# Kernel tuning notes

Measured on AMD Instinct MI355X. Metric: run time of the kernel, lower is better.

The kernel has to match this reference:

```python
import jax, jax.numpy as jnp
import numpy as np

D_MODEL = 1024
N_HEADS = 16
HEAD_DIM = D_MODEL // N_HEADS
BS, SEQ = 4, 2048


def setup_inputs() -> dict:
    key = jax.random.key(0)
    ks = jax.random.split(key, 12)
    s = 1.0 / np.sqrt(D_MODEL)
    inp = {
        'query': jax.random.normal(ks[0], (BS, SEQ, D_MODEL), jnp.float32),
        'key_in': jax.random.normal(ks[1], (BS, SEQ, D_MODEL), jnp.float32),
        'value': jax.random.normal(ks[2], (BS, SEQ, D_MODEL), jnp.float32),
        'mask': jax.random.randint(ks[3], (BS, SEQ, SEQ), 0, 2, jnp.int32),
        'wq_w': jax.random.uniform(ks[4], (D_MODEL, D_MODEL), jnp.float32, -s, s),
        'wq_b': jax.random.uniform(ks[5], (D_MODEL,), jnp.float32, -s, s),
        'wk_w': jax.random.uniform(ks[6], (D_MODEL, D_MODEL), jnp.float32, -s, s),
        'wk_b': jax.random.uniform(ks[7], (D_MODEL,), jnp.float32, -s, s),
        'wv_w': jax.random.uniform(ks[8], (D_MODEL, D_MODEL), jnp.float32, -s, s),
        'wv_b': jax.random.uniform(ks[9], (D_MODEL,), jnp.float32, -s, s),
        'fc_w': jax.random.uniform(ks[10], (D_MODEL, D_MODEL), jnp.float32, -s, s),
        'fc_b': jax.random.uniform(ks[11], (D_MODEL,), jnp.float32, -s, s),
    }
    return inp


def _split_heads(x):
    # [B, S, D] -> [B, H, S, Dh]
    b, s, _ = x.shape
    return x.reshape(b, s, N_HEADS, HEAD_DIM).transpose(0, 2, 1, 3)


def reference(query, key_in, value, mask,
              wq_w, wq_b, wk_w, wk_b, wv_w, wv_b, fc_w, fc_b):
    # torch Linear: y = x @ W.T + b
    q = _split_heads(query @ wq_w.T + wq_b)   # [B,H,S,Dh]
    k = _split_heads(key_in @ wk_w.T + wk_b)
    v = _split_heads(value @ wv_w.T + wv_b)

    scale = 1.0 / np.sqrt(HEAD_DIM).astype(np.float32)
    scores = jnp.einsum('bhqd,bhkd->bhqk', q, k) * scale  # [B,H,S,S]
    m = (mask[:, None, :, :] == 0)
    scores = jnp.where(m, jnp.float32(-1e9), scores)
    attn = jax.nn.softmax(scores, axis=-1)
    out = jnp.einsum('bhqk,bhkd->bhqd', attn, v)           # [B,H,S,Dh]
    out = out.transpose(0, 2, 1, 3).reshape(query.shape[0], query.shape[1], D_MODEL)
    return out @ fc_w.T + fc_b
```

## Files before the change

### kernel.cpp

```cpp
#include <hip/hip_runtime.h>
#include <hip/hip_bf16.h>


typedef __attribute__((ext_vector_type(8))) short bf16x8;
typedef __attribute__((ext_vector_type(4))) float f32x4;
typedef unsigned int u32;
typedef unsigned short u16;
typedef unsigned long long u64;

#define SEQ 2048
#define DM 1024
#define NH 16
#define HD 64

__device__ __forceinline__ u16 f2bf(float f) {
  __hip_bfloat16 h = __float2bfloat16(f);
  return __builtin_bit_cast(u16, h);
}
__device__ __forceinline__ u32 pack2(float a, float b) {
  return (u32)f2bf(a) | ((u32)f2bf(b) << 16);
}
__device__ __forceinline__ float max3f(float a, float b, float c) {
  return fmaxf(fmaxf(a, b), c);
}

typedef __attribute__((address_space(3))) u32 lds_u32;
typedef const __attribute__((address_space(1))) u32 gbl_u32;
__device__ __forceinline__ void gll16(const void* g, void* l) {
  __builtin_amdgcn_global_load_lds((gbl_u32*)g, (lds_u32*)l, 16, 0, 0);
}

__global__ __launch_bounds__(256) void cast_all(
    const float* __restrict__ q, const float* __restrict__ k, const float* __restrict__ v,
    const float* __restrict__ wq, const float* __restrict__ wk,
    const float* __restrict__ wv, const float* __restrict__ wf,
    u16* __restrict__ dst)
{
  int i4 = blockIdx.x * 256 + threadIdx.x;
  const float* s; int rel;
  if      (i4 < 2097152) { s = q;  rel = i4;           }
  else if (i4 < 4194304) { s = k;  rel = i4 - 2097152; }
  else if (i4 < 6291456) { s = v;  rel = i4 - 4194304; }
  else if (i4 < 6553600) { s = wq; rel = i4 - 6291456; }
  else if (i4 < 6815744) { s = wk; rel = i4 - 6553600; }
  else if (i4 < 7077888) { s = wv; rel = i4 - 6815744; }
  else                   { s = wf; rel = i4 - 7077888; }
  float4 val = ((const float4*)s)[rel];
  uint2 o; o.x = pack2(val.x, val.y); o.y = pack2(val.z, val.w);
  ((uint2*)dst)[i4] = o;
}

__global__ __launch_bounds__(256) void maskbits(const int* __restrict__ mask, u32* __restrict__ bm) {
  int t = blockIdx.x * 256 + threadIdx.x;
  int v = mask[t];
  u64 bal = __ballot(v != 0);
  if ((threadIdx.x & 63) == 0) {
    bm[(t >> 5)]     = (u32)bal;
    bm[(t >> 5) + 1] = (u32)(bal >> 32);
  }
}

template<int MODE>
__global__ __launch_bounds__(256) void gemm_bt(
    const u16* __restrict__ Pm, const u16* __restrict__ Pn,
    const float* __restrict__ bias, void* __restrict__ outp, float scale)
{
  __shared__ alignas(16) u16 Al[128 * 32];
  __shared__ alignas(16) u16 Bl[128 * 32];
  const int tid = threadIdx.x;
  const int l = tid & 63;
  const int wv = tid >> 6;
  const int lane15 = l & 15, g = l >> 4;
  const int wr = wv >> 1, wc = wv & 1;
  const int mBase = blockIdx.y * 128, nBase = blockIdx.x * 128;

  f32x4 acc[4][4];
#pragma unroll
  for (int a = 0; a < 4; ++a)
#pragma unroll
    for (int b = 0; b < 4; ++b) acc[a][b] = (f32x4){0.f, 0.f, 0.f, 0.f};

  const int srow = tid >> 2, skc = tid & 3;
  const u16* gA = Pm + (size_t)(mBase + srow) * 1024 + skc * 8;
  const u16* gB = Pn + (size_t)(nBase + srow) * 1024 + skc * 8;

  for (int kt = 0; kt < 32; ++kt) {
    __syncthreads();
    const u16* a0 = gA + kt * 32;
    const u16* b0 = gB + kt * 32;
    gll16(a0,             &Al[tid * 8]);
    gll16(a0 + 64 * 1024, &Al[(tid + 256) * 8]);
    gll16(b0,             &Bl[tid * 8]);
    gll16(b0 + 64 * 1024, &Bl[(tid + 256) * 8]);
    __syncthreads();
    bf16x8 af[4], bff[4];
#pragma unroll
    for (int mt = 0; mt < 4; ++mt)
      af[mt] = *(const bf16x8*)&Al[(wr * 64 + mt * 16 + lane15) * 32 + g * 8];
#pragma unroll
    for (int nt = 0; nt < 4; ++nt)
      bff[nt] = *(const bf16x8*)&Bl[(wc * 64 + nt * 16 + lane15) * 32 + g * 8];
#pragma unroll
    for (int mt = 0; mt < 4; ++mt)
#pragma unroll
      for (int nt = 0; nt < 4; ++nt)
        acc[mt][nt] = __builtin_amdgcn_mfma_f32_16x16x32_bf16(af[mt], bff[nt], acc[mt][nt], 0, 0, 0);
  }

#pragma unroll
  for (int mt = 0; mt < 4; ++mt) {
    const int mi = mBase + wr * 64 + mt * 16 + g * 4;
#pragma unroll
    for (int nt = 0; nt < 4; ++nt) {
      const int ni = nBase + wc * 64 + nt * 16 + lane15;
      f32x4 v = acc[mt][nt];
      if constexpr (MODE == 0) {
        f32x4 bb = *(const f32x4*)&bias[mi];
        int b = ni >> 11, s = ni & 2047;
        int h = mi >> 6, dh = mi & 63;
        uint2 w;
        w.x = pack2((v[0] + bb[0]) * scale, (v[1] + bb[1]) * scale);
        w.y = pack2((v[2] + bb[2]) * scale, (v[3] + bb[3]) * scale);
        *(uint2*)&((u16*)outp)[((size_t)((b << 4) + h) * SEQ + s) * HD + dh] = w;
      } else if constexpr (MODE == 1) {
        float bv = bias[ni];
        int b = mi >> 11, s = mi & 2047;
        int h = ni >> 6, dh = ni & 63;
        uint2 w;
        w.x = pack2(v[0] + bv, v[1] + bv);
        w.y = pack2(v[2] + bv, v[3] + bv);
        *(uint2*)&((u16*)outp)[((size_t)((b << 4) + h) * HD + dh) * SEQ + s] = w;
      } else {
        f32x4 bb = *(const f32x4*)&bias[mi];
        f32x4 w = v + bb;
        *(f32x4*)&((float*)outp)[(size_t)ni * 1024 + mi] = w;
      }
    }
  }
}

__global__ __launch_bounds__(256) void attn_kernel(
    const u16* __restrict__ Qb, const u16* __restrict__ Kb,
    const u16* __restrict__ Vt, const u32* __restrict__ bm,
    u16* __restrict__ AO)
{
  __shared__ alignas(16) u16 Kl[2][64 * 64];
  __shared__ alignas(16) u16 Vl[2][64 * 64];
  __shared__ uint2 Pl[4][256];
  const int bid = blockIdx.x;
  const int bh = (bid & 7) * 8 + ((bid >> 3) & 7);
  const int qt = bid >> 6;
  const int b = bh >> 4, h = bh & 15;
  const int tid = threadIdx.x;
  const int wv = tid >> 6, l = tid & 63;
  const int q16 = l & 15, g = l >> 4;
  const int lr = l >> 3, lc = l & 7;
  const int sx = q16 & 7;

  const u16* Qp = Qb + (size_t)bh * SEQ * HD;
  const u16* Kp = Kb + (size_t)bh * SEQ * HD;
  const u16* Vp = Vt + (size_t)bh * HD * SEQ;
  const int qrow = qt * 64 + wv * 16;

  const bf16x8 qf0 = *(const bf16x8*)&Qp[(qrow + q16) * HD + g * 8];
  const bf16x8 qf1 = *(const bf16x8*)&Qp[(qrow + q16) * HD + 32 + g * 8];
  const u32* bmq = bm + (size_t)(b * SEQ + qrow + q16) * (SEQ / 32);

  const int i0 = wv * 2;
  const u16* ksrc0 = Kp + (size_t)((i0 + 0) * 8 + lr) * HD + (lc ^ lr) * 8;
  const u16* ksrc1 = Kp + (size_t)((i0 + 1) * 8 + lr) * HD + (lc ^ lr) * 8;
  const u16* vsrc0 = Vp + (size_t)((i0 + 0) * 8 + lr) * SEQ + (lc ^ lr) * 8;
  const u16* vsrc1 = Vp + (size_t)((i0 + 1) * 8 + lr) * SEQ + (lc ^ lr) * 8;

  union { u32 u[4]; bf16x8 v; } ones;
  ones.u[0] = ones.u[1] = ones.u[2] = ones.u[3] = 0x3F803F80u;

  float mrun = 8.0f;
  f32x4 accO[4], accSum;
#pragma unroll
  for (int dt = 0; dt < 4; ++dt) accO[dt] = (f32x4){0.f, 0.f, 0.f, 0.f};
  accSum = (f32x4){0.f, 0.f, 0.f, 0.f};
  const f32x4 z = {0.f, 0.f, 0.f, 0.f};

  {
    gll16(ksrc0, &Kl[0][(i0 + 0) * 512 + l * 8]);
    gll16(ksrc1, &Kl[0][(i0 + 1) * 512 + l * 8]);
    gll16(vsrc0, &Vl[0][(i0 + 0) * 512 + l * 8]);
    gll16(vsrc1, &Vl[0][(i0 + 1) * 512 + l * 8]);
  }

  for (int kb = 0; kb < SEQ / 64; ++kb) {
    const int cur = kb & 1;
    const u32 w0 = bmq[kb * 2], w1 = bmq[kb * 2 + 1];
    if (kb < SEQ / 64 - 1) {
      const int nxt = cur ^ 1;
      const size_t ko = (size_t)(kb + 1) * 64;
      gll16(ksrc0 + ko * HD, &Kl[nxt][(i0 + 0) * 512 + l * 8]);
      gll16(ksrc1 + ko * HD, &Kl[nxt][(i0 + 1) * 512 + l * 8]);
      gll16(vsrc0 + ko,      &Vl[nxt][(i0 + 0) * 512 + l * 8]);
      gll16(vsrc1 + ko,      &Vl[nxt][(i0 + 1) * 512 + l * 8]);
      asm volatile("s_waitcnt vmcnt(4)" ::: "memory");
    } else {
      asm volatile("s_waitcnt vmcnt(0)" ::: "memory");
    }
    __builtin_amdgcn_s_barrier();
    __builtin_amdgcn_sched_barrier(0);

    const u16* Kc = &Kl[cur][0];
    const u16* Vc = &Vl[cur][0];

    f32x4 accS[4];
    __builtin_amdgcn_s_setprio(1);
#pragma unroll
    for (int n = 0; n < 4; ++n) {
      const int rk = n * 16 + q16;
      bf16x8 kf0 = *(const bf16x8*)&Kc[rk * 64 + ((g ^ sx) * 8)];
      bf16x8 kf1 = *(const bf16x8*)&Kc[rk * 64 + (((4 + g) ^ sx) * 8)];
      accS[n] = __builtin_amdgcn_mfma_f32_16x16x32_bf16(kf0, qf0, z, 0, 0, 0);
      accS[n] = __builtin_amdgcn_mfma_f32_16x16x32_bf16(kf1, qf1, accS[n], 0, 0, 0);
    }
    __builtin_amdgcn_s_setprio(0);

    float s[16];
#pragma unroll
    for (int n = 0; n < 4; ++n) {
      const u32 nib = ((n & 2) ? w1 : w0) >> ((n & 1) * 16 + g * 4);
#pragma unroll
      for (int r = 0; r < 4; ++r)
        s[n * 4 + r] = ((nib >> r) & 1u) ? accS[n][r] : -1e9f;
    }
    float pmax;
    {
      float g0 = max3f(s[0],  s[1],  s[2]);
      float g1 = max3f(s[3],  s[4],  s[5]);
      float g2 = max3f(s[6],  s[7],  s[8]);
      float g3 = max3f(s[9],  s[10], s[11]);
      float g4 = max3f(s[12], s[13], s[14]);
      pmax = max3f(max3f(g0, g1, g2), max3f(g3, g4, s[15]), -INFINITY);
    }
    pmax = fmaxf(pmax, __shfl_xor(pmax, 16));
    pmax = fmaxf(pmax, __shfl_xor(pmax, 32));

    if (!__all(pmax - mrun <= 12.0f)) {
      const float mnew = fmaxf(mrun, pmax);
      const float alpha = exp2f(mrun - mnew);
      accSum[0] *= alpha;
#pragma unroll
      for (int dt = 0; dt < 4; ++dt) {
        accO[dt][0] *= alpha; accO[dt][1] *= alpha;
        accO[dt][2] *= alpha; accO[dt][3] *= alpha;
      }
      mrun = mnew;
    }

    u16 pb[16];
#pragma unroll
    for (int i = 0; i < 16; ++i)
      pb[i] = f2bf(exp2f(s[i] - mrun));

#pragma unroll
    for (int n = 0; n < 4; ++n) {
      uint2 pw;
      pw.x = (u32)pb[n * 4 + 0] | ((u32)pb[n * 4 + 1] << 16);
      pw.y = (u32)pb[n * 4 + 2] | ((u32)pb[n * 4 + 3] << 16);
      Pl[wv][q16 * 16 + ((n * 4 + g) ^ q16)] = pw;
    }
#pragma unroll
    for (int ch = 0; ch < 2; ++ch) {
      const int u0 = ch * 8 + g * 2;
      uint2 lo = Pl[wv][q16 * 16 + ((u0 + 0) ^ q16)];
      uint2 hi = Pl[wv][q16 * 16 + ((u0 + 1) ^ q16)];
      union { u32 u[4]; bf16x8 v; } pf;
      pf.u[0] = lo.x; pf.u[1] = lo.y; pf.u[2] = hi.x; pf.u[3] = hi.y;
      __builtin_amdgcn_s_setprio(1);
#pragma unroll
      for (int dt = 0; dt < 4; ++dt) {
        const int rv = dt * 16 + q16;
        bf16x8 vf = *(const bf16x8*)&Vc[rv * 64 + (((ch * 4 + g) ^ sx) * 8)];
        accO[dt] = __builtin_amdgcn_mfma_f32_16x16x32_bf16(vf, pf.v, accO[dt], 0, 0, 0);
      }
      accSum = __builtin_amdgcn_mfma_f32_16x16x32_bf16(ones.v, pf.v, accSum, 0, 0, 0);
      __builtin_amdgcn_s_setprio(0);
    }
    __builtin_amdgcn_s_barrier();
  }

  const float inv = 1.f / fmaxf(accSum[0], 1e-37f);
#pragma unroll
  for (int dt = 0; dt < 4; ++dt) {
    uint2 o;
    o.x = pack2(accO[dt][0] * inv, accO[dt][1] * inv);
    o.y = pack2(accO[dt][2] * inv, accO[dt][3] * inv);
    *(uint2*)&AO[(size_t)(b * SEQ + qrow + q16) * DM + h * HD + dt * 16 + g * 4] = o;
  }
}

extern "C" void kernel_launch(void* const* d_in, const int* in_sizes, int n_in,
                              void* d_out, int out_size, void* d_ws, size_t ws_size,
                              hipStream_t stream) {
  const float* q  = (const float*)d_in[0];
  const float* k  = (const float*)d_in[1];
  const float* v  = (const float*)d_in[2];
  const int* mask = (const int*)d_in[3];
  const float* wq = (const float*)d_in[4];
  const float* bq = (const float*)d_in[5];
  const float* wk = (const float*)d_in[6];
  const float* bk = (const float*)d_in[7];
  const float* wv = (const float*)d_in[8];
  const float* bv = (const float*)d_in[9];
  const float* wf = (const float*)d_in[10];
  const float* bf = (const float*)d_in[11];

  u16* XQ = (u16*)d_ws;
  u16* XK = XQ + 8388608;
  u16* XV = XK + 8388608;
  u16* WQ = XV + 8388608;
  u16* WK = WQ + 1048576;
  u16* WV = WK + 1048576;
  u16* WF = WV + 1048576;
  u16* QB = WF + 1048576;
  u16* KB = QB + 8388608;
  u16* VT = KB + 8388608;
  u32* BM = (u32*)(VT + 8388608);
  u16* AO = XQ;

  const float qscale = 0.125f * 1.44269504088896f;

  cast_all<<<28672, 256, 0, stream>>>(q, k, v, wq, wk, wv, wf, XQ);
  maskbits<<<65536, 256, 0, stream>>>(mask, BM);
  gemm_bt<0><<<dim3(64, 8), 256, 0, stream>>>(WQ, XQ, bq, QB, qscale);
  gemm_bt<0><<<dim3(64, 8), 256, 0, stream>>>(WK, XK, bk, KB, 1.0f);
  gemm_bt<1><<<dim3(8, 64), 256, 0, stream>>>(XV, WV, bv, VT, 1.0f);
  attn_kernel<<<2048, 256, 0, stream>>>(QB, KB, VT, BM, AO);
  gemm_bt<2><<<dim3(64, 8), 256, 0, stream>>>(WF, AO, bf, (float*)d_out, 1.0f);
}
```

Measured before the change: 487.7 us.

## Batch QKV projections into one launch, use packed bf16 convert, trim attention loop

Merges the three Q/K/V projection GEMMs into one launch with a z-dimension selecting operands, and splits the output projection into its own kernel. Float-to-bf16 conversion now uses a single packed v_cvt_pk_bf16_f32 instruction. The attention loop drops its s_setprio calls, works on the score accumulators in place, advances K/V source pointers incrementally, and adds an occupancy hint to launch bounds. The aim is fewer launches, better GPU fill during projections, and fewer conversion and address instructions, at the cost of possible register-pressure or scheduling changes.

```diff
diff --git a/kernel.cpp b/kernel.cpp
--- a/kernel.cpp
+++ b/kernel.cpp
@@ -13,12 +13,10 @@
 #define NH 16
 #define HD 64
 
-__device__ __forceinline__ u16 f2bf(float f) {
-  __hip_bfloat16 h = __float2bfloat16(f);
-  return __builtin_bit_cast(u16, h);
-}
 __device__ __forceinline__ u32 pack2(float a, float b) {
-  return (u32)f2bf(a) | ((u32)f2bf(b) << 16);
+  u32 d;
+  asm("v_cvt_pk_bf16_f32 %0, %1, %2" : "=v"(d) : "v"(a), "v"(b));
+  return d;
 }
 __device__ __forceinline__ float max3f(float a, float b, float c) {
   return fmaxf(fmaxf(a, b), c);
@@ -60,19 +58,26 @@
   }
 }
 
-template<int MODE>
-__global__ __launch_bounds__(256) void gemm_bt(
-    const u16* __restrict__ Pm, const u16* __restrict__ Pn,
-    const float* __restrict__ bias, void* __restrict__ outp, float scale)
+__global__ __launch_bounds__(256) void gemm_qkv(
+    const u16* __restrict__ WQp, const u16* __restrict__ XQp, const float* __restrict__ bq,
+    const u16* __restrict__ WKp, const u16* __restrict__ XKp, const float* __restrict__ bk,
+    const u16* __restrict__ WVp, const u16* __restrict__ XVp, const float* __restrict__ bv,
+    u16* __restrict__ QB, u16* __restrict__ KB, u16* __restrict__ VT, float qscale)
 {
   __shared__ alignas(16) u16 Al[128 * 32];
   __shared__ alignas(16) u16 Bl[128 * 32];
+  const int z = blockIdx.z;
+  const u16 *Pm, *Pn; const float* bias;
+  int mBase, nBase;
+  if (z == 0)      { Pm = WQp; Pn = XQp; bias = bq; mBase = blockIdx.y * 128; nBase = blockIdx.x * 128; }
+  else if (z == 1) { Pm = WKp; Pn = XKp; bias = bk; mBase = blockIdx.y * 128; nBase = blockIdx.x * 128; }
+  else             { Pm = XVp; Pn = WVp; bias = bv; mBase = blockIdx.x * 128; nBase = blockIdx.y * 128; }
+
   const int tid = threadIdx.x;
   const int l = tid & 63;
   const int wv = tid >> 6;
   const int lane15 = l & 15, g = l >> 4;
   const int wr = wv >> 1, wc = wv & 1;
-  const int mBase = blockIdx.y * 128, nBase = blockIdx.x * 128;
 
   f32x4 acc[4][4];
 #pragma unroll
@@ -107,39 +112,105 @@
         acc[mt][nt] = __builtin_amdgcn_mfma_f32_16x16x32_bf16(af[mt], bff[nt], acc[mt][nt], 0, 0, 0);
   }
 
-#pragma unroll
-  for (int mt = 0; mt < 4; ++mt) {
-    const int mi = mBase + wr * 64 + mt * 16 + g * 4;
-#pragma unroll
-    for (int nt = 0; nt < 4; ++nt) {
-      const int ni = nBase + wc * 64 + nt * 16 + lane15;
-      f32x4 v = acc[mt][nt];
-      if constexpr (MODE == 0) {
-        f32x4 bb = *(const f32x4*)&bias[mi];
+  if (z <= 1) {
+    const float scale = (z == 0) ? qscale : 1.0f;
+    u16* outp = (z == 0) ? QB : KB;
+#pragma unroll
+    for (int mt = 0; mt < 4; ++mt) {
+      const int mi = mBase + wr * 64 + mt * 16 + g * 4;
+      f32x4 bb = *(const f32x4*)&bias[mi];
+#pragma unroll
+      for (int nt = 0; nt < 4; ++nt) {
+        const int ni = nBase + wc * 64 + nt * 16 + lane15;
+        f32x4 v = acc[mt][nt];
         int b = ni >> 11, s = ni & 2047;
         int h = mi >> 6, dh = mi & 63;
         uint2 w;
         w.x = pack2((v[0] + bb[0]) * scale, (v[1] + bb[1]) * scale);
         w.y = pack2((v[2] + bb[2]) * scale, (v[3] + bb[3]) * scale);
-        *(uint2*)&((u16*)outp)[((size_t)((b << 4) + h) * SEQ + s) * HD + dh] = w;
-      } else if constexpr (MODE == 1) {
-        float bv = bias[ni];
+        *(uint2*)&outp[((size_t)((b << 4) + h) * SEQ + s) * HD + dh] = w;
+      }
+    }
+  } else {
+#pragma unroll
+    for (int mt = 0; mt < 4; ++mt) {
+      const int mi = mBase + wr * 64 + mt * 16 + g * 4;
+#pragma unroll
+      for (int nt = 0; nt < 4; ++nt) {
+        const int ni = nBase + wc * 64 + nt * 16 + lane15;
+        float bvv = bias[ni];
+        f32x4 v = acc[mt][nt];
         int b = mi >> 11, s = mi & 2047;
         int h = ni >> 6, dh = ni & 63;
         uint2 w;
-        w.x = pack2(v[0] + bv, v[1] + bv);
-        w.y = pack2(v[2] + bv, v[3] + bv);
-        *(uint2*)&((u16*)outp)[((size_t)((b << 4) + h) * HD + dh) * SEQ + s] = w;
-      } else {
-        f32x4 bb = *(const f32x4*)&bias[mi];
-        f32x4 w = v + bb;
-        *(f32x4*)&((float*)outp)[(size_t)ni * 1024 + mi] = w;
+        w.x = pack2(v[0] + bvv, v[1] + bvv);
+        w.y = pack2(v[2] + bvv, v[3] + bvv);
+        *(uint2*)&VT[((size_t)((b << 4) + h) * HD + dh) * SEQ + s] = w;
       }
     }
   }
 }
 
-__global__ __launch_bounds__(256) void attn_kernel(
+__global__ __launch_bounds__(256) void gemm_fc(
+    const u16* __restrict__ Pm, const u16* __restrict__ Pn,
+    const float* __restrict__ bias, float* __restrict__ outp)
+{
+  __shared__ alignas(16) u16 Al[128 * 32];
+  __shared__ alignas(16) u16 Bl[128 * 32];
+  const int tid = threadIdx.x;
+  const int l = tid & 63;
+  const int wv = tid >> 6;
+  const int lane15 = l & 15, g = l >> 4;
+  const int wr = wv >> 1, wc = wv & 1;
+  const int mBase = blockIdx.y * 128, nBase = blockIdx.x * 128;
+
+  f32x4 acc[4][4];
+#pragma unroll
+  for (int a = 0; a < 4; ++a)
+#pragma unroll
+    for (int b = 0; b < 4; ++b) acc[a][b] = (f32x4){0.f, 0.f, 0.f, 0.f};
+
+  const int srow = tid >> 2, skc = tid & 3;
+  const u16* gA = Pm + (size_t)(mBase + srow) * 1024 + skc * 8;
+  const u16* gB = Pn + (size_t)(nBase + srow) * 1024 + skc * 8;
+
+  for (int kt = 0; kt < 32; ++kt) {
+    __syncthreads();
+    const u16* a0 = gA + kt * 32;
+    const u16* b0 = gB + kt * 32;
+    gll16(a0,             &Al[tid * 8]);
+    gll16(a0 + 64 * 1024, &Al[(tid + 256) * 8]);
+    gll16(b0,             &Bl[tid * 8]);
+    gll16(b0 + 64 * 1024, &Bl[(tid + 256) * 8]);
+    __syncthreads();
+    bf16x8 af[4], bff[4];
+#pragma unroll
+    for (int mt = 0; mt < 4; ++mt)
+      af[mt] = *(const bf16x8*)&Al[(wr * 64 + mt * 16 + lane15) * 32 + g * 8];
+#pragma unroll
+    for (int nt = 0; nt < 4; ++nt)
+      bff[nt] = *(const bf16x8*)&Bl[(wc * 64 + nt * 16 + lane15) * 32 + g * 8];
+#pragma unroll
+    for (int mt = 0; mt < 4; ++mt)
+#pragma unroll
+      for (int nt = 0; nt < 4; ++nt)
+        acc[mt][nt] = __builtin_amdgcn_mfma_f32_16x16x32_bf16(af[mt], bff[nt], acc[mt][nt], 0, 0, 0);
+  }
+
+#pragma unroll
+  for (int mt = 0; mt < 4; ++mt) {
+    const int mi = mBase + wr * 64 + mt * 16 + g * 4;
+    f32x4 bb = *(const f32x4*)&bias[mi];
+#pragma unroll
+    for (int nt = 0; nt < 4; ++nt) {
+      const int ni = nBase + wc * 64 + nt * 16 + lane15;
+      f32x4 w = acc[mt][nt] + bb;
+      *(f32x4*)&outp[(size_t)ni * 1024 + mi] = w;
+    }
+  }
+}
+
+__global__ __launch_bounds__(256, 4) void attn_kernel(
     const u16* __restrict__ Qb, const u16* __restrict__ Kb,
     const u16* __restrict__ Vt, const u32* __restrict__ bm,
     u16* __restrict__ AO)
@@ -167,10 +238,10 @@
   const u32* bmq = bm + (size_t)(b * SEQ + qrow + q16) * (SEQ / 32);
 
   const int i0 = wv * 2;
-  const u16* ksrc0 = Kp + (size_t)((i0 + 0) * 8 + lr) * HD + (lc ^ lr) * 8;
-  const u16* ksrc1 = Kp + (size_t)((i0 + 1) * 8 + lr) * HD + (lc ^ lr) * 8;
-  const u16* vsrc0 = Vp + (size_t)((i0 + 0) * 8 + lr) * SEQ + (lc ^ lr) * 8;
-  const u16* vsrc1 = Vp + (size_t)((i0 + 1) * 8 + lr) * SEQ + (lc ^ lr) * 8;
+  const u16* ks0 = Kp + (size_t)((i0 + 0) * 8 + lr) * HD + (lc ^ lr) * 8;
+  const u16* ks1 = Kp + (size_t)((i0 + 1) * 8 + lr) * HD + (lc ^ lr) * 8;
+  const u16* vs0 = Vp + (size_t)((i0 + 0) * 8 + lr) * SEQ + (lc ^ lr) * 8;
+  const u16* vs1 = Vp + (size_t)((i0 + 1) * 8 + lr) * SEQ + (lc ^ lr) * 8;
 
   union { u32 u[4]; bf16x8 v; } ones;
   ones.u[0] = ones.u[1] = ones.u[2] = ones.u[3] = 0x3F803F80u;
@@ -182,23 +253,22 @@
   accSum = (f32x4){0.f, 0.f, 0.f, 0.f};
   const f32x4 z = {0.f, 0.f, 0.f, 0.f};
 
-  {
-    gll16(ksrc0, &Kl[0][(i0 + 0) * 512 + l * 8]);
-    gll16(ksrc1, &Kl[0][(i0 + 1) * 512 + l * 8]);
-    gll16(vsrc0, &Vl[0][(i0 + 0) * 512 + l * 8]);
-    gll16(vsrc1, &Vl[0][(i0 + 1) * 512 + l * 8]);
-  }
+  gll16(ks0, &Kl[0][(i0 + 0) * 512 + l * 8]);
+  gll16(ks1, &Kl[0][(i0 + 1) * 512 + l * 8]);
+  gll16(vs0, &Vl[0][(i0 + 0) * 512 + l * 8]);
+  gll16(vs1, &Vl[0][(i0 + 1) * 512 + l * 8]);
+  ks0 += 64 * HD; ks1 += 64 * HD; vs0 += 64; vs1 += 64;
 
   for (int kb = 0; kb < SEQ / 64; ++kb) {
     const int cur = kb & 1;
     const u32 w0 = bmq[kb * 2], w1 = bmq[kb * 2 + 1];
     if (kb < SEQ / 64 - 1) {
       const int nxt = cur ^ 1;
-      const size_t ko = (size_t)(kb + 1) * 64;
-      gll16(ksrc0 + ko * HD, &Kl[nxt][(i0 + 0) * 512 + l * 8]);
-      gll16(ksrc1 + ko * HD, &Kl[nxt][(i0 + 1) * 512 + l * 8]);
-      gll16(vsrc0 + ko,      &Vl[nxt][(i0 + 0) * 512 + l * 8]);
-      gll16(vsrc1 + ko,      &Vl[nxt][(i0 + 1) * 512 + l * 8]);
+      gll16(ks0, &Kl[nxt][(i0 + 0) * 512 + l * 8]);
+      gll16(ks1, &Kl[nxt][(i0 + 1) * 512 + l * 8]);
+      gll16(vs0, &Vl[nxt][(i0 + 0) * 512 + l * 8]);
+      gll16(vs1, &Vl[nxt][(i0 + 1) * 512 + l * 8]);
+      ks0 += 64 * HD; ks1 += 64 * HD; vs0 += 64; vs1 += 64;
       asm volatile("s_waitcnt vmcnt(4)" ::: "memory");
     } else {
       asm volatile("s_waitcnt vmcnt(0)" ::: "memory");
@@ -210,7 +280,6 @@
     const u16* Vc = &Vl[cur][0];
 
     f32x4 accS[4];
-    __builtin_amdgcn_s_setprio(1);
 #pragma unroll
     for (int n = 0; n < 4; ++n) {
       const int rk = n * 16 + q16;
@@ -219,25 +288,21 @@
       accS[n] = __builtin_amdgcn_mfma_f32_16x16x32_bf16(kf0, qf0, z, 0, 0, 0);
       accS[n] = __builtin_amdgcn_mfma_f32_16x16x32_bf16(kf1, qf1, accS[n], 0, 0, 0);
     }
-    __builtin_amdgcn_s_setprio(0);
-
-    float s[16];
+
 #pragma unroll
     for (int n = 0; n < 4; ++n) {
       const u32 nib = ((n & 2) ? w1 : w0) >> ((n & 1) * 16 + g * 4);
 #pragma unroll
       for (int r = 0; r < 4; ++r)
-        s[n * 4 + r] = ((nib >> r) & 1u) ? accS[n][r] : -1e9f;
-    }
-    float pmax;
-    {
-      float g0 = max3f(s[0],  s[1],  s[2]);
-      float g1 = max3f(s[3],  s[4],  s[5]);
-      float g2 = max3f(s[6],  s[7],  s[8]);
-      float g3 = max3f(s[9],  s[10], s[11]);
-      float g4 = max3f(s[12], s[13], s[14]);
-      pmax = max3f(max3f(g0, g1, g2), max3f(g3, g4, s[15]), -INFINITY);
-    }
+        accS[n][r] = ((nib >> r) & 1u) ? accS[n][r] : -1e9f;
+    }
+
+    float t0 = max3f(accS[0][0], accS[0][1], accS[0][2]);
+    float t1 = max3f(accS[0][3], accS[1][0], accS[1][1]);
+    float t2 = max3f(accS[1][2], accS[1][3], accS[2][0]);
+    float t3 = max3f(accS[2][1], accS[2][2], accS[2][3]);
+    float t4 = max3f(accS[3][0], accS[3][1], accS[3][2]);
+    float pmax = fmaxf(max3f(t0, t1, t2), max3f(t3, t4, accS[3][3]));
     pmax = fmaxf(pmax, __shfl_xor(pmax, 16));
     pmax = fmaxf(pmax, __shfl_xor(pmax, 32));
 
@@ -253,16 +318,13 @@
       mrun = mnew;
     }
 
-    u16 pb[16];
-#pragma unroll
-    for (int i = 0; i < 16; ++i)
-      pb[i] = f2bf(exp2f(s[i] - mrun));
-
 #pragma unroll
     for (int n = 0; n < 4; ++n) {
-      uint2 pw;
-      pw.x = (u32)pb[n * 4 + 0] | ((u32)pb[n * 4 + 1] << 16);
-      pw.y = (u32)pb[n * 4 + 2] | ((u32)pb[n * 4 + 3] << 16);
+      float p0 = exp2f(accS[n][0] - mrun);
+      float p1 = exp2f(accS[n][1] - mrun);
+      float p2 = exp2f(accS[n][2] - mrun);
+      float p3 = exp2f(accS[n][3] - mrun);
+      uint2 pw; pw.x = pack2(p0, p1); pw.y = pack2(p2, p3);
       Pl[wv][q16 * 16 + ((n * 4 + g) ^ q16)] = pw;
     }
 #pragma unroll
@@ -272,7 +334,6 @@
       uint2 hi = Pl[wv][q16 * 16 + ((u0 + 1) ^ q16)];
       union { u32 u[4]; bf16x8 v; } pf;
       pf.u[0] = lo.x; pf.u[1] = lo.y; pf.u[2] = hi.x; pf.u[3] = hi.y;
-      __builtin_amdgcn_s_setprio(1);
 #pragma unroll
       for (int dt = 0; dt < 4; ++dt) {
         const int rv = dt * 16 + q16;
@@ -280,7 +341,6 @@
         accO[dt] = __builtin_amdgcn_mfma_f32_16x16x32_bf16(vf, pf.v, accO[dt], 0, 0, 0);
       }
       accSum = __builtin_amdgcn_mfma_f32_16x16x32_bf16(ones.v, pf.v, accSum, 0, 0, 0);
-      __builtin_amdgcn_s_setprio(0);
     }
     __builtin_amdgcn_s_barrier();
   }
@@ -328,9 +388,8 @@
 
   cast_all<<<28672, 256, 0, stream>>>(q, k, v, wq, wk, wv, wf, XQ);
   maskbits<<<65536, 256, 0, stream>>>(mask, BM);
-  gemm_bt<0><<<dim3(64, 8), 256, 0, stream>>>(WQ, XQ, bq, QB, qscale);
-  gemm_bt<0><<<dim3(64, 8), 256, 0, stream>>>(WK, XK, bk, KB, 1.0f);
-  gemm_bt<1><<<dim3(8, 64), 256, 0, stream>>>(XV, WV, bv, VT, 1.0f);
+  gemm_qkv<<<dim3(64, 8, 3), 256, 0, stream>>>(WQ, XQ, bq, WK, XK, bk, WV, XV, bv,
+                                               QB, KB, VT, qscale);
   attn_kernel<<<2048, 256, 0, stream>>>(QB, KB, VT, BM, AO);
-  gemm_bt<2><<<dim3(64, 8), 256, 0, stream>>>(WF, AO, bf, (float*)d_out, 1.0f);
-}
+  gemm_fc<<<dim3(64, 8), 256, 0, stream>>>(WF, AO, bf, (float*)d_out);
+}
```

After: 472.6 us. -3.1%, faster.
